# Kernel tuning notes

Hardware: AMD Instinct MI355X
Metric: run time of the kernel (lower is better)

## Reference

```python
import jax, jax.numpy as jnp
import numpy as np

H = 1024       # hidden_size
R = 4          # downsacale_ratio -> bottleneck H//R = 256
DI = 2048      # mamba d_inner = expand * H
NS = 16        # d_state
KC = 4         # d_conv
DTR = 64       # dt_rank = ceil(H/16)
B, L = 4, 1024


def setup_inputs() -> dict:
    key = jax.random.key(0)
    ks = iter(jax.random.split(key, 32))
    w = lambda shape, s=0.02: jax.random.normal(next(ks), shape, jnp.float32) * s
    Hr = H // R
    inp = {
        'x': jax.random.normal(next(ks), (B, L, H), jnp.float32),
        't': jax.random.normal(next(ks), (B, H), jnp.float32),
        # adaLN modulation: SiLU -> Linear(H, 3H)
        'ada_w': w((H, 3 * H)), 'ada_b': jnp.zeros((3 * H,), jnp.float32),
        # hg_dense: Linear(H,H/R) SiLU Linear(H/R,H)
        'hgd_w1': w((H, Hr)), 'hgd_b1': jnp.zeros((Hr,), jnp.float32),
        'hgd_w2': w((Hr, H)), 'hgd_b2': jnp.zeros((H,), jnp.float32),
        # Mamba params
        'in_proj_w': w((H, 2 * DI)),
        'conv_w': w((DI, KC), 0.1), 'conv_b': jnp.zeros((DI,), jnp.float32),
        'x_proj_w': w((DI, DTR + 2 * NS)),
        'dt_proj_w': w((DTR, DI), 0.1),
        'dt_proj_b': jnp.log(jnp.expm1(jnp.full((DI,), 0.01, jnp.float32))),  # softplus^-1(0.01)
        'A_log': jnp.log(jnp.broadcast_to(jnp.arange(1, NS + 1, dtype=jnp.float32), (DI, NS))),
        'Dp': jnp.ones((DI,), jnp.float32),
        'out_proj_w': w((DI, H)),
        # hg_fuse
        'fm_w': w((H, Hr)), 'fm_b': jnp.zeros((Hr,), jnp.float32),
        'fr_w': w((H, Hr)), 'fr_b': jnp.zeros((Hr,), jnp.float32),
        'ff_w': w((Hr, H)), 'ff_b': jnp.zeros((H,), jnp.float32),
    }
    return inp


def _ln(x, eps=1e-6):
    mu = jnp.mean(x, -1, keepdims=True)
    var = jnp.mean(jnp.square(x - mu), -1, keepdims=True)
    return (x - mu) / jnp.sqrt(var + eps)


def _mamba(xd, in_proj_w, conv_w, conv_b, x_proj_w, dt_proj_w, dt_proj_b, A_log, Dp, out_proj_w):
    # xd: [B, L, H]
    xz = xd @ in_proj_w                      # [B, L, 2*DI]
    xm, z = jnp.split(xz, 2, axis=-1)
    # causal depthwise conv over time
    xc = jnp.swapaxes(xm, 1, 2)              # [B, DI, L]
    xc = jax.lax.conv_general_dilated(
        xc, conv_w[:, None, :], window_strides=(1,), padding=[(KC - 1, 0)],
        feature_group_count=DI, dimension_numbers=('NCH', 'OIH', 'NCH'))
    xc = jax.nn.silu(jnp.swapaxes(xc, 1, 2) + conv_b)   # [B, L, DI]
    dbl = xc @ x_proj_w                      # [B, L, DTR + 2*NS]
    dt = jax.nn.softplus(dbl[..., :DTR] @ dt_proj_w + dt_proj_b)   # [B, L, DI]
    Bm = dbl[..., DTR:DTR + NS]              # [B, L, NS]
    Cm = dbl[..., DTR + NS:]                 # [B, L, NS]
    A = -jnp.exp(A_log)                      # [DI, NS]

    def step(h, inp):
        dt_t, x_t, B_t, C_t = inp            # [B,DI],[B,DI],[B,NS],[B,NS]
        dA = jnp.exp(dt_t[:, :, None] * A)                       # [B, DI, NS]
        h = dA * h + (dt_t * x_t)[:, :, None] * B_t[:, None, :]
        y = jnp.einsum('bdn,bn->bd', h, C_t)
        return h, y

    h0 = jnp.zeros((xd.shape[0], DI, NS), xd.dtype)
    seq = (jnp.moveaxis(dt, 1, 0), jnp.moveaxis(xc, 1, 0),
           jnp.moveaxis(Bm, 1, 0), jnp.moveaxis(Cm, 1, 0))
    _, ys = jax.lax.scan(step, h0, seq)
    y = jnp.moveaxis(ys, 0, 1) + xc * Dp     # [B, L, DI]
    y = y * jax.nn.silu(z)
    return y @ out_proj_w                    # [B, L, H]


def reference(x, t, ada_w, ada_b, hgd_w1, hgd_b1, hgd_w2, hgd_b2,
              in_proj_w, conv_w, conv_b, x_proj_w, dt_proj_w, dt_proj_b,
              A_log, Dp, out_proj_w, fm_w, fm_b, fr_w, fr_b, ff_w, ff_b):
    ada = jax.nn.silu(t) @ ada_w + ada_b               # [B, 3H]
    shift, scale, alpha = jnp.split(ada, 3, axis=-1)
    x1 = _ln(x) * (1 + scale[:, None, :]) + shift[:, None, :]
    xd = jax.nn.silu(x1 @ hgd_w1 + hgd_b1) @ hgd_w2 + hgd_b2
    x1_2 = _mamba(xd, in_proj_w, conv_w, conv_b, x_proj_w, dt_proj_w,
                  dt_proj_b, A_log, Dp, out_proj_w)
    a = jax.nn.silu(x1_2 @ fm_w + fm_b)
    b = jax.nn.silu(x1 @ fr_w + fr_b)
    fuse = (a * b) @ ff_w + ff_b
    return x + alpha[:, None, :] * fuse
```

## Files before the change

kernel.cpp:

```cpp
#include <hip/hip_runtime.h>
#include <math.h>
#include <stdint.h>

#define H_   1024
#define HR_  256
#define DI_  2048
#define NS_  16
#define KC_  4
#define DTR_ 64
#define B_   4
#define L_   1024
#define ROWS (B_*L_)
#define H3_  3072
#define NCH_ 16
#define CL_  64
#define CLT_ 8

typedef short bf16x8 __attribute__((ext_vector_type(8)));
typedef float f32x4  __attribute__((ext_vector_type(4)));

__device__ __forceinline__ float silu_f(float v) { return v / (1.f + __expf(-v)); }

__device__ __forceinline__ uint32_t pack_bf16_2(float a, float b) {
    uint32_t ua = __float_as_uint(a);
    uint32_t ub = __float_as_uint(b);
    uint32_t ra = (ua + 0x7FFFu + ((ua >> 16) & 1u)) >> 16;
    uint32_t rb = (ub + 0x7FFFu + ((ub >> 16) & 1u)) >> 16;
    return ra | (rb << 16);
}
__device__ __forceinline__ unsigned short cvt_bf16(float a) {
    uint32_t ua = __float_as_uint(a);
    return (unsigned short)((ua + 0x7FFFu + ((ua >> 16) & 1u)) >> 16);
}
__device__ __forceinline__ float bf16_to_f(unsigned short u) {
    return __uint_as_float(((uint32_t)u) << 16);
}

__device__ __forceinline__ void gload16(const short* g, short* l) {
    __builtin_amdgcn_global_load_lds(
        (const __attribute__((address_space(1))) void*)g,
        (__attribute__((address_space(3))) void*)l, 16, 0, 0);
}

#define TW_HGDFR 0ull
#define TW_HGD2  524288ull
#define TW_INPJ  786432ull
#define TW_XPJ   4980736ull
#define TW_DTPJ  5242880ull
#define TW_OPJ   5373952ull
#define TW_FM    7471104ull
#define TW_FF    7733248ull
#define TWT      7995392ull

__global__ __launch_bounds__(256) void wtrans_kernel(
    const float* __restrict__ s0, const float* __restrict__ s1,
    const float* __restrict__ s2, const float* __restrict__ s3,
    const float* __restrict__ s4, const float* __restrict__ s5,
    const float* __restrict__ s6, const float* __restrict__ s7,
    const float* __restrict__ s8, short* __restrict__ wt)
{
    int bid = blockIdx.x;
    const float* src; short* dst; int K, N, rel;
    if      (bid < 256)  { src = s0; dst = wt + TW_HGDFR;          K = 1024; N = 256;  rel = bid; }
    else if (bid < 512)  { src = s1; dst = wt + TW_HGDFR + 262144; K = 1024; N = 256;  rel = bid - 256; }
    else if (bid < 768)  { src = s2; dst = wt + TW_HGD2;           K = 256;  N = 1024; rel = bid - 512; }
    else if (bid < 4864) { src = s3; dst = wt + TW_INPJ;           K = 1024; N = 4096; rel = bid - 768; }
    else if (bid < 5120) { src = s4; dst = wt + TW_XPJ;            K = 2048; N = 96;   rel = bid - 4864; }
    else if (bid < 5248) { src = s5; dst = wt + TW_DTPJ;           K = 64;   N = 2048; rel = bid - 5120; }
    else if (bid < 7296) { src = s6; dst = wt + TW_OPJ;            K = 2048; N = 1024; rel = bid - 5248; }
    else if (bid < 7552) { src = s7; dst = wt + TW_FM;             K = 1024; N = 256;  rel = bid - 7296; }
    else                 { src = s8; dst = wt + TW_FF;             K = 256;  N = 1024; rel = bid - 7552; }
    int tkc = K >> 5;
    int tk = rel % tkc, tn = rel / tkc;

    __shared__ float ld[32][33];
    int tx = threadIdx.x & 7, ty = threadIdx.x >> 3;
    int kk = tk * 32 + ty, nn = tn * 32 + tx * 4;
    float4 v = make_float4(0.f, 0.f, 0.f, 0.f);
    if (nn < N) v = *(const float4*)&src[(size_t)kk * N + nn];
    ld[ty][tx * 4 + 0] = v.x; ld[ty][tx * 4 + 1] = v.y;
    ld[ty][tx * 4 + 2] = v.z; ld[ty][tx * 4 + 3] = v.w;
    __syncthreads();
    int nn2 = tn * 32 + ty, kk2 = tk * 32 + tx * 4;
    float a0 = ld[tx * 4 + 0][ty], a1 = ld[tx * 4 + 1][ty];
    float a2 = ld[tx * 4 + 2][ty], a3 = ld[tx * 4 + 3][ty];
    uint2 p = { pack_bf16_2(a0, a1), pack_bf16_2(a2, a3) };
    *(uint2*)&dst[(size_t)nn2 * K + kk2] = p;
}

__global__ __launch_bounds__(256) void cwt_kernel(
    const float* __restrict__ conv_w, float* __restrict__ cwt)
{
    int d = blockIdx.x * 256 + threadIdx.x;
    float4 v = *(const float4*)&conv_w[d * KC_];
    cwt[0 * DI_ + d] = v.x;
    cwt[1 * DI_ + d] = v.y;
    cwt[2 * DI_ + d] = v.z;
    cwt[3 * DI_ + d] = v.w;
}

__global__ __launch_bounds__(256) void ada_kernel(
    const float* __restrict__ t, const float* __restrict__ ada_w,
    const float* __restrict__ ada_b, float* __restrict__ ada)
{
    int b   = blockIdx.y;
    int col = blockIdx.x * 256 + threadIdx.x;
    __shared__ float st[H_];
    for (int i = threadIdx.x; i < H_; i += 256) {
        float v = t[b * H_ + i];
        st[i] = silu_f(v);
    }
    __syncthreads();
    float acc = 0.f;
    for (int k = 0; k < H_; ++k)
        acc = fmaf(st[k], ada_w[(size_t)k * H3_ + col], acc);
    ada[b * H3_ + col] = acc + ada_b[col];
}

__global__ __launch_bounds__(256) void ln_mod_kernel(
    const float* __restrict__ x, const float* __restrict__ ada,
    short* __restrict__ x1b)
{
    int row = blockIdx.x;
    int b   = row >> 10;
    const float* xr = x + (size_t)row * H_;
    float4 v = ((const float4*)xr)[threadIdx.x];
    float s  = v.x + v.y + v.z + v.w;
    float s2 = v.x*v.x + v.y*v.y + v.z*v.z + v.w*v.w;

    __shared__ float red[8];
    int wave = threadIdx.x >> 6, lane = threadIdx.x & 63;
    #pragma unroll
    for (int off = 32; off; off >>= 1) {
        s  += __shfl_down(s,  off);
        s2 += __shfl_down(s2, off);
    }
    if (lane == 0) { red[wave] = s; red[4 + wave] = s2; }
    __syncthreads();
    float ts  = red[0] + red[1] + red[2] + red[3];
    float ts2 = red[4] + red[5] + red[6] + red[7];
    float mu  = ts  * (1.f / H_);
    float var = ts2 * (1.f / H_) - mu * mu;
    float inv = rsqrtf(var + 1e-6f);

    const float* sh = ada + b * H3_;
    int i = threadIdx.x * 4;
    float4 sh4 = *(const float4*)&sh[i];
    float4 sc4 = *(const float4*)&sh[H_ + i];
    float ox = (v.x - mu) * inv * (1.f + sc4.x) + sh4.x;
    float oy = (v.y - mu) * inv * (1.f + sc4.y) + sh4.y;
    float oz = (v.z - mu) * inv * (1.f + sc4.z) + sh4.z;
    float ow = (v.w - mu) * inv * (1.f + sc4.w) + sh4.w;
    uint2 p = { pack_bf16_2(ox, oy), pack_bf16_2(oz, ow) };
    *(uint2*)(x1b + (size_t)row * H_ + i) = p;
}

template<int ACT, bool SPLITK>
__global__ __launch_bounds__(256) void gemm128(
    const short* __restrict__ A, int lda,
    const short* __restrict__ Wt, int ldw,
    const float* __restrict__ bias,
    float* __restrict__ C, short* __restrict__ Cb, short* __restrict__ Cb2,
    int ldc, int M, int N, int K,
    const float* __restrict__ E0, const float* __restrict__ E1)
{
    __shared__ short As[3][4096];
    __shared__ short Bs[3][4096];
    int tid  = threadIdx.x;
    int lane = tid & 63, wv = tid >> 6, wm = wv >> 1, wn = wv & 1;
    int n0 = blockIdx.x * 128;
    int m0 = blockIdx.y * 128;

    if (SPLITK) {
        int z = blockIdx.z;
        A  += (size_t)z * K;
        Wt += (size_t)z * K;
        C  += (size_t)z * M * N;
    }

    int r = lane & 15, g = lane >> 4;
    int sA = wv * 2;
    const short* ga0 = A  + (size_t)(m0 + sA * 16 + r) * lda + g * 8;
    const short* ga1 = ga0 + (size_t)16 * lda;
    const short* gb0 = Wt + (size_t)(n0 + sA * 16 + r) * ldw + g * 8;
    const short* gb1 = gb0 + (size_t)16 * ldw;

    f32x4 acc[4][4];
    #pragma unroll
    for (int i = 0; i < 4; ++i)
        #pragma unroll
        for (int j = 0; j < 4; ++j) {
            acc[i][j][0] = 0.f; acc[i][j][1] = 0.f;
            acc[i][j][2] = 0.f; acc[i][j][3] = 0.f;
        }

    #define STAGE(buf, koff)                                    \
        do {                                                    \
            gload16(ga0 + (koff), &As[buf][sA * 512]);          \
            gload16(ga1 + (koff), &As[buf][sA * 512 + 512]);    \
            gload16(gb0 + (koff), &Bs[buf][sA * 512]);          \
            gload16(gb1 + (koff), &Bs[buf][sA * 512 + 512]);    \
        } while (0)

    #define COMPUTE(buf)                                                          \
        do {                                                                      \
            bf16x8 af[4], bfr[4];                                                 \
            _Pragma("unroll")                                                     \
            for (int i = 0; i < 4; ++i)                                           \
                af[i] = *(const bf16x8*)&As[buf][(wm * 4 + i) * 512 + lane * 8];  \
            _Pragma("unroll")                                                     \
            for (int j = 0; j < 4; ++j)                                           \
                bfr[j] = *(const bf16x8*)&Bs[buf][(wn * 4 + j) * 512 + lane * 8]; \
            _Pragma("unroll")                                                     \
            for (int i = 0; i < 4; ++i)                                           \
                _Pragma("unroll")                                                 \
                for (int j = 0; j < 4; ++j)                                       \
                    acc[i][j] = __builtin_amdgcn_mfma_f32_16x16x32_bf16(          \
                        af[i], bfr[j], acc[i][j], 0, 0, 0);                       \
        } while (0)

    int T = K >> 5;
    STAGE(0, 0);
    if (T > 1) STAGE(1, 32);
    for (int t = 0; t < T; ++t) {
        if (t + 1 < T) asm volatile("s_waitcnt vmcnt(4)" ::: "memory");
        else           asm volatile("s_waitcnt vmcnt(0)" ::: "memory");
        __builtin_amdgcn_s_barrier();
        if (t + 2 < T) STAGE((t + 2) % 3, (t + 2) * 32);
        COMPUTE(t % 3);
    }
    #undef STAGE
    #undef COMPUTE

    #pragma unroll
    for (int i = 0; i < 4; ++i) {
        int mb = m0 + wm * 64 + i * 16 + ((lane >> 4) << 2);
        #pragma unroll
        for (int j = 0; j < 4; ++j) {
            int n = n0 + wn * 64 + j * 16 + (lane & 15);
            if (n < N) {
                float bv;
                if (ACT == 6) bv = (n < 256) ? bias[n] : E0[n - 256];
                else          bv = bias ? bias[n] : 0.f;
                #pragma unroll
                for (int rr = 0; rr < 4; ++rr) {
                    int m = mb + rr;
                    float v = acc[i][j][rr] + bv;
                    size_t ci = (size_t)m * ldc + n;
                    if (ACT == 6) {
                        float sv = silu_f(v);
                        if (n < 256) Cb[(size_t)m * 256 + n]        = (short)cvt_bf16(sv);
                        else         Cb2[(size_t)m * 256 + (n-256)] = (short)cvt_bf16(sv);
                    } else {
                        if (ACT == 2) v = (v > 20.f) ? v : log1pf(__expf(v));
                        else if (ACT == 4) {
                            int bb = m >> 10;
                            v = E0[ci] + E1[bb * H3_ + 2 * H_ + n] * v;
                        }
                        if (C)  C[ci]  = v;
                        if (Cb) Cb[ci] = (short)cvt_bf16(v);
                    }
                }
            }
        }
    }
}

template<int ACT>
__global__ __launch_bounds__(512) void gemm256(
    const short* __restrict__ A, int lda,
    const short* __restrict__ Wt, int ldw,
    short* __restrict__ Cb, int M, int N, int K)
{
    extern __shared__ short lds[];
    short* Asb = lds;
    short* Bsb = lds + 24576;
    int tid  = threadIdx.x;
    int lane = tid & 63, wv = tid >> 6;
    int wm = wv >> 2, wn = wv & 3;
    int n0 = blockIdx.x * 256;
    int m0 = blockIdx.y * 256;

    int r = lane & 15, g = lane >> 4;
    int sA = wv * 2;
    const short* ga0 = A  + (size_t)(m0 + sA * 16 + r) * lda + g * 8;
    const short* ga1 = ga0 + (size_t)16 * lda;
    const short* gb0 = Wt + (size_t)(n0 + sA * 16 + r) * ldw + g * 8;
    const short* gb1 = gb0 + (size_t)16 * ldw;

    f32x4 acc[8][4];
    #pragma unroll
    for (int i = 0; i < 8; ++i)
        #pragma unroll
        for (int j = 0; j < 4; ++j) {
            acc[i][j][0] = 0.f; acc[i][j][1] = 0.f;
            acc[i][j][2] = 0.f; acc[i][j][3] = 0.f;
        }

    #define STAGE2(buf, koff)                                       \
        do {                                                        \
            gload16(ga0 + (koff), &Asb[(buf) * 8192 + sA * 512]);   \
            gload16(ga1 + (koff), &Asb[(buf) * 8192 + sA * 512 + 512]); \
            gload16(gb0 + (koff), &Bsb[(buf) * 8192 + sA * 512]);   \
            gload16(gb1 + (koff), &Bsb[(buf) * 8192 + sA * 512 + 512]); \
        } while (0)

    int T = K >> 5;
    STAGE2(0, 0);
    if (T > 1) STAGE2(1, 32);
    for (int t = 0; t < T; ++t) {
        if (t + 1 < T) asm volatile("s_waitcnt vmcnt(4)" ::: "memory");
        else           asm volatile("s_waitcnt vmcnt(0)" ::: "memory");
        __builtin_amdgcn_s_barrier();
        if (t + 2 < T) STAGE2((t + 2) % 3, (t + 2) * 32);
        {
            int buf = t % 3;
            bf16x8 af[8], bfr[4];
            #pragma unroll
            for (int i = 0; i < 8; ++i)
                af[i] = *(const bf16x8*)&Asb[buf * 8192 + (wm * 8 + i) * 512 + lane * 8];
            #pragma unroll
            for (int j = 0; j < 4; ++j)
                bfr[j] = *(const bf16x8*)&Bsb[buf * 8192 + (wn * 4 + j) * 512 + lane * 8];
            __builtin_amdgcn_s_setprio(1);
            #pragma unroll
            for (int i = 0; i < 8; ++i)
                #pragma unroll
                for (int j = 0; j < 4; ++j)
                    acc[i][j] = __builtin_amdgcn_mfma_f32_16x16x32_bf16(
                        af[i], bfr[j], acc[i][j], 0, 0, 0);
            __builtin_amdgcn_s_setprio(0);
        }
    }
    #undef STAGE2

    #pragma unroll
    for (int i = 0; i < 8; ++i) {
        int mb = m0 + wm * 128 + i * 16 + ((lane >> 4) << 2);
        #pragma unroll
        for (int j = 0; j < 4; ++j) {
            int n = n0 + wn * 64 + j * 16 + (lane & 15);
            #pragma unroll
            for (int rr = 0; rr < 4; ++rr) {
                int m = mb + rr;
                float v = acc[i][j][rr];
                if (ACT == 5) {
                    size_t idx = (n < DI_) ? ((size_t)m * DI_ + n)
                                           : ((size_t)ROWS * DI_ + (size_t)m * DI_ + (n - DI_));
                    Cb[idx] = (short)cvt_bf16(v);
                }
            }
        }
    }
}

__global__ __launch_bounds__(256) void redk_xproj(
    const float* __restrict__ part, float* __restrict__ dbl,
    short* __restrict__ dblb)
{
    size_t i = ((size_t)blockIdx.x * 256 + threadIdx.x) * 4;
    const size_t seg = (size_t)ROWS * 96;
    float4 s = *(const float4*)(part + i);
    #pragma unroll
    for (int z = 1; z < 8; ++z) {
        float4 p = *(const float4*)(part + z * seg + i);
        s.x += p.x; s.y += p.y; s.z += p.z; s.w += p.w;
    }
    *(float4*)(dbl + i) = s;
    uint2 p = { pack_bf16_2(s.x, s.y), pack_bf16_2(s.z, s.w) };
    *(uint2*)(dblb + i) = p;
}

__global__ __launch_bounds__(256) void redk_op(
    const float* __restrict__ part, short* __restrict__ x12b)
{
    size_t i = ((size_t)blockIdx.x * 256 + threadIdx.x) * 4;
    const size_t seg = (size_t)ROWS * H_;
    float4 a = *(const float4*)(part + i);
    float4 b = *(const float4*)(part + seg + i);
    uint2 p = { pack_bf16_2(a.x + b.x, a.y + b.y), pack_bf16_2(a.z + b.z, a.w + b.w) };
    *(uint2*)(x12b + i) = p;
}

__global__ __launch_bounds__(256) void redk_fm(
    const float* __restrict__ part, const float* __restrict__ fm_b,
    const short* __restrict__ frlin, short* __restrict__ abb)
{
    size_t i = ((size_t)blockIdx.x * 256 + threadIdx.x) * 4;
    const size_t seg = (size_t)ROWS * HR_;
    float4 s = *(const float4*)(part + i);
    #pragma unroll
    for (int z = 1; z < 4; ++z) {
        float4 p = *(const float4*)(part + z * seg + i);
        s.x += p.x; s.y += p.y; s.z += p.z; s.w += p.w;
    }
    int col = (int)(i & (HR_ - 1));
    float4 b = *(const float4*)(fm_b + col);
    const short* fr = frlin + i;
    float o0 = silu_f(s.x + b.x) * bf16_to_f((unsigned short)fr[0]);
    float o1 = silu_f(s.y + b.y) * bf16_to_f((unsigned short)fr[1]);
    float o2 = silu_f(s.z + b.z) * bf16_to_f((unsigned short)fr[2]);
    float o3 = silu_f(s.w + b.w) * bf16_to_f((unsigned short)fr[3]);
    uint2 p = { pack_bf16_2(o0, o1), pack_bf16_2(o2, o3) };
    *(uint2*)(abb + i) = p;
}

__global__ __launch_bounds__(256) void conv_kernel(
    const short* __restrict__ xmb, const float* __restrict__ cwt,
    const float* __restrict__ conv_b, short* __restrict__ xcb)
{
    int d0 = threadIdx.x * 8;
    int b  = blockIdx.y;
    int l0 = blockIdx.x * CLT_;

    float w[KC_][8];
    #pragma unroll
    for (int j = 0; j < KC_; ++j) {
        float4 a = *(const float4*)&cwt[j * DI_ + d0];
        float4 c = *(const float4*)&cwt[j * DI_ + d0 + 4];
        w[j][0] = a.x; w[j][1] = a.y; w[j][2] = a.z; w[j][3] = a.w;
        w[j][4] = c.x; w[j][5] = c.y; w[j][6] = c.z; w[j][7] = c.w;
    }
    float bia[8];
    {
        float4 b0 = *(const float4*)&conv_b[d0];
        float4 b1 = *(const float4*)&conv_b[d0 + 4];
        bia[0] = b0.x; bia[1] = b0.y; bia[2] = b0.z; bia[3] = b0.w;
        bia[4] = b1.x; bia[5] = b1.y; bia[6] = b1.z; bia[7] = b1.w;
    }

    const short* base = xmb + (size_t)b * L_ * DI_ + d0;
    short*       outb = xcb + (size_t)b * L_ * DI_ + d0;

    bf16x8 win[KC_];
    #pragma unroll
    for (int j = 0; j < KC_ - 1; ++j) {
        int ll = l0 - (KC_ - 1) + j;
        if (ll >= 0) win[j] = *(const bf16x8*)(base + (size_t)ll * DI_);
        else         win[j] = (bf16x8)0;
    }
    for (int l = l0; l < l0 + CLT_; ++l) {
        win[KC_ - 1] = *(const bf16x8*)(base + (size_t)l * DI_);
        bf16x8 o;
        #pragma unroll
        for (int e = 0; e < 8; ++e) {
            float acc = bia[e];
            #pragma unroll
            for (int j = 0; j < KC_; ++j)
                acc = fmaf(bf16_to_f((unsigned short)win[j][e]), w[j][e], acc);
            o[e] = (short)cvt_bf16(silu_f(acc));
        }
        *(bf16x8*)(outb + (size_t)l * DI_) = o;
        win[0] = win[1]; win[1] = win[2]; win[2] = win[3];
    }
}

__global__ __launch_bounds__(256) void scan_part1(
    const short* __restrict__ dtb, const short* __restrict__ xcb,
    const float* __restrict__ dbl, const float* __restrict__ A_log,
    float* __restrict__ hend, float* __restrict__ dtsum)
{
    int bx = blockIdx.x;
    int dg = bx & 7;
    int bc = bx >> 3;
    int c  = bc & (NCH_ - 1);
    int b  = bc >> 4;
    int d  = dg * 256 + threadIdx.x;

    float Aa[NS_];
    #pragma unroll
    for (int n = 0; n < NS_; ++n) Aa[n] = -__expf(A_log[d * NS_ + n]);

    __shared__ float sB[CL_][NS_];
    for (int idx = threadIdx.x; idx < CL_ * NS_; idx += 256) {
        int l = idx >> 4, n = idx & 15;
        sB[l][n] = dbl[(size_t)(b * L_ + c * CL_ + l) * 96 + DTR_ + n];
    }
    __syncthreads();

    float h[NS_];
    #pragma unroll
    for (int n = 0; n < NS_; ++n) h[n] = 0.f;
    float sdt = 0.f;

    for (int l = 0; l < CL_; ++l) {
        size_t off = (size_t)(b * L_ + c * CL_ + l) * DI_ + d;
        float dtv = bf16_to_f((unsigned short)dtb[off]);
        float xv  = bf16_to_f((unsigned short)xcb[off]);
        float du  = dtv * xv;
        sdt += dtv;
        #pragma unroll
        for (int n = 0; n < NS_; ++n)
            h[n] = fmaf(__expf(dtv * Aa[n]), h[n], du * sB[l][n]);
    }
    #pragma unroll
    for (int n = 0; n < NS_; ++n)
        hend[((size_t)((b * NCH_ + c) * NS_ + n)) * DI_ + d] = h[n];
    dtsum[(size_t)(b * NCH_ + c) * DI_ + d] = sdt;
}

__global__ __launch_bounds__(256) void scan_part2(
    const short* __restrict__ dtb, const short* __restrict__ xcb,
    const short* __restrict__ zb, const float* __restrict__ dbl,
    const float* __restrict__ A_log, const float* __restrict__ Dp,
    const float* __restrict__ hend, const float* __restrict__ dtsum,
    short* __restrict__ y2b)
{
    int bx = blockIdx.x;
    int dg = bx & 7;
    int bc = bx >> 3;
    int c  = bc & (NCH_ - 1);
    int b  = bc >> 4;
    int d  = dg * 256 + threadIdx.x;

    float Aa[NS_];
    #pragma unroll
    for (int n = 0; n < NS_; ++n) Aa[n] = -__expf(A_log[d * NS_ + n]);

    __shared__ float sBC[CL_][2 * NS_];
    for (int idx = threadIdx.x; idx < CL_ * 2 * NS_; idx += 256) {
        int l = idx >> 5, n = idx & 31;
        sBC[l][n] = dbl[(size_t)(b * L_ + c * CL_ + l) * 96 + DTR_ + n];
    }
    __syncthreads();

    float h[NS_];
    #pragma unroll
    for (int n = 0; n < NS_; ++n) h[n] = 0.f;
    for (int j = 0; j < c; ++j) {
        float s = dtsum[(size_t)(b * NCH_ + j) * DI_ + d];
        #pragma unroll
        for (int n = 0; n < NS_; ++n)
            h[n] = fmaf(__expf(Aa[n] * s), h[n],
                        hend[((size_t)((b * NCH_ + j) * NS_ + n)) * DI_ + d]);
    }

    float Dpv = Dp[d];
    for (int l = 0; l < CL_; ++l) {
        size_t row = (size_t)(b * L_ + c * CL_ + l);
        size_t off = row * DI_ + d;
        float dtv = bf16_to_f((unsigned short)dtb[off]);
        float xv  = bf16_to_f((unsigned short)xcb[off]);
        float zv  = bf16_to_f((unsigned short)zb[off]);
        float du  = dtv * xv;
        float y = 0.f;
        #pragma unroll
        for (int n = 0; n < NS_; ++n) {
            float dA = __expf(dtv * Aa[n]);
            h[n] = fmaf(dA, h[n], du * sBC[l][n]);
            y = fmaf(h[n], sBC[l][NS_ + n], y);
        }
        y = fmaf(xv, Dpv, y);
        y2b[off] = (short)cvt_bf16(y * silu_f(zv));
    }
}

extern "C" void kernel_launch(void* const* d_in, const int* in_sizes, int n_in,
                              void* d_out, int out_size, void* d_ws, size_t ws_size,
                              hipStream_t stream)
{
    const float* x         = (const float*)d_in[0];
    const float* t         = (const float*)d_in[1];
    const float* ada_w     = (const float*)d_in[2];
    const float* ada_b     = (const float*)d_in[3];
    const float* hgd_w1    = (const float*)d_in[4];
    const float* hgd_b1    = (const float*)d_in[5];
    const float* hgd_w2    = (const float*)d_in[6];
    const float* hgd_b2    = (const float*)d_in[7];
    const float* in_proj_w = (const float*)d_in[8];
    const float* conv_w    = (const float*)d_in[9];
    const float* conv_b    = (const float*)d_in[10];
    const float* x_proj_w  = (const float*)d_in[11];
    const float* dt_proj_w = (const float*)d_in[12];
    const float* dt_proj_b = (const float*)d_in[13];
    const float* A_log     = (const float*)d_in[14];
    const float* Dp        = (const float*)d_in[15];
    const float* out_proj_w= (const float*)d_in[16];
    const float* fm_w      = (const float*)d_in[17];
    const float* fm_b      = (const float*)d_in[18];
    const float* fr_w      = (const float*)d_in[19];
    const float* fr_b      = (const float*)d_in[20];
    const float* ff_w      = (const float*)d_in[21];
    const float* ff_b      = (const float*)d_in[22];
    float* out = (float*)d_out;

    char* p = (char*)d_ws;
    auto alloc = [&](size_t bytes) { char* r = p; p += (bytes + 255) & ~255ull; return r; };

    short* wt      = (short*)alloc(TWT * 2);
    float* cwt     = (float*)alloc((size_t)KC_ * DI_ * 4);
    short* x1b     = (short*)alloc((size_t)ROWS * H_ * 2);
    short* h1b     = (short*)alloc((size_t)ROWS * HR_ * 2);
    short* frlin   = (short*)alloc((size_t)ROWS * HR_ * 2);
    short* xdb     = (short*)alloc((size_t)ROWS * H_ * 2);
    short* xmzb    = (short*)alloc((size_t)ROWS * DI_ * 4);
    short* xcb     = (short*)alloc((size_t)ROWS * DI_ * 2);
    short* y2b     = (short*)alloc((size_t)ROWS * DI_ * 2);
    short* dtb     = (short*)alloc((size_t)ROWS * DI_ * 2);
    float* bigpart = (float*)alloc((size_t)2 * ROWS * H_ * 4);
    float* dbl     = (float*)alloc((size_t)ROWS * 96 * 4);
    short* dblb    = (short*)alloc((size_t)ROWS * 96 * 2);
    short* x12b    = (short*)alloc((size_t)ROWS * H_ * 2);
    short* abb     = (short*)alloc((size_t)ROWS * HR_ * 2);
    float* ada     = (float*)alloc((size_t)B_ * H3_ * 4);

    short* xmb   = xmzb;
    short* zb    = xmzb + (size_t)ROWS * DI_;
    float* hend  = (float*)x12b;
    float* dtsum = (float*)abb;

    dim3 blk(256), b512(512);

    wtrans_kernel<<<dim3(7808), blk, 0, stream>>>(
        hgd_w1, fr_w, hgd_w2, in_proj_w, x_proj_w, dt_proj_w, out_proj_w,
        fm_w, ff_w, wt);
    cwt_kernel<<<dim3(DI_ / 256), blk, 0, stream>>>(conv_w, cwt);
    ada_kernel<<<dim3(H3_ / 256, B_), blk, 0, stream>>>(t, ada_w, ada_b, ada);
    ln_mod_kernel<<<dim3(ROWS), blk, 0, stream>>>(x, ada, x1b);
    gemm128<6, false><<<dim3(4, 32), blk, 0, stream>>>(
        x1b, H_, wt + TW_HGDFR, H_, hgd_b1, nullptr, h1b, frlin,
        512, ROWS, 512, H_, fr_b, nullptr);
    gemm128<0, false><<<dim3(8, 32), blk, 0, stream>>>(
        h1b, HR_, wt + TW_HGD2, HR_, hgd_b2, nullptr, xdb, nullptr,
        H_, ROWS, H_, HR_, nullptr, nullptr);
    gemm256<5><<<dim3(16, 16), b512, 98304, stream>>>(
        xdb, H_, wt + TW_INPJ, H_, xmb, ROWS, 2 * DI_, H_);
    conv_kernel<<<dim3(L_ / CLT_, B_), blk, 0, stream>>>(xmb, cwt, conv_b, xcb);
    gemm128<0, true><<<dim3(1, 32, 8), blk, 0, stream>>>(
        xcb, DI_, wt + TW_XPJ, DI_, nullptr, bigpart, nullptr, nullptr,
        96, ROWS, 96, 256, nullptr, nullptr);
    redk_xproj<<<dim3(ROWS * 96 / 4 / 256), blk, 0, stream>>>(bigpart, dbl, dblb);
    gemm128<2, false><<<dim3(16, 32), blk, 0, stream>>>(
        dblb, 96, wt + TW_DTPJ, DTR_, dt_proj_b, nullptr, dtb, nullptr,
        DI_, ROWS, DI_, DTR_, nullptr, nullptr);
    scan_part1<<<dim3(B_ * NCH_ * 8), blk, 0, stream>>>(
        dtb, xcb, dbl, A_log, hend, dtsum);
    scan_part2<<<dim3(B_ * NCH_ * 8), blk, 0, stream>>>(
        dtb, xcb, zb, dbl, A_log, Dp, hend, dtsum, y2b);
    gemm128<0, true><<<dim3(8, 32, 2), blk, 0, stream>>>(
        y2b, DI_, wt + TW_OPJ, DI_, nullptr, bigpart, nullptr, nullptr,
        H_, ROWS, H_, 1024, nullptr, nullptr);
    redk_op<<<dim3(ROWS * H_ / 4 / 256), blk, 0, stream>>>(bigpart, x12b);
    gemm128<0, true><<<dim3(2, 32, 4), blk, 0, stream>>>(
        x12b, H_, wt + TW_FM, H_, nullptr, bigpart, nullptr, nullptr,
        HR_, ROWS, HR_, 256, nullptr, nullptr);
    redk_fm<<<dim3(ROWS * HR_ / 4 / 256), blk, 0, stream>>>(bigpart, fm_b, frlin, abb);
    gemm128<4, false><<<dim3(8, 32), blk, 0, stream>>>(
        abb, HR_, wt + TW_FF, HR_, ff_b, out, nullptr, nullptr,
        H_, ROWS, H_, HR_, x, ada);
}
```

Baseline: 404.6 us.

## Split scan state across thread pairs and add a separate inter-chunk prefix kernel

The chunked selective scan now assigns two threads per channel, each owning 8 of the 16 state entries. This doubles the block count and halves per-thread register and exp work, and the two halves of y are combined with a shuffle. The sequential inter-chunk carry, which each part-2 block used to recompute over all earlier chunks, moves into a new scan_mid kernel that writes the starting state of every chunk once. The cost is an extra kernel launch, duplicated dt/x/z loads across each thread pair, and the hin buffer reusing bigpart memory.

Result: no change. 409.0 us (+1.1%).

```diff
diff --git a/kernel.cpp b/kernel.cpp
--- a/kernel.cpp
+++ b/kernel.cpp
@@ -461,15 +461,18 @@
     float* __restrict__ hend, float* __restrict__ dtsum)
 {
     int bx = blockIdx.x;
-    int dg = bx & 7;
-    int bc = bx >> 3;
+    int dg = bx & 15;
+    int bc = bx >> 4;
     int c  = bc & (NCH_ - 1);
     int b  = bc >> 4;
-    int d  = dg * 256 + threadIdx.x;
-
-    float Aa[NS_];
-    #pragma unroll
-    for (int n = 0; n < NS_; ++n) Aa[n] = -__expf(A_log[d * NS_ + n]);
+    int tid  = threadIdx.x;
+    int d    = dg * 128 + (tid >> 1);
+    int half = tid & 1;
+    int n0   = half * 8;
+
+    float Aa[8];
+    #pragma unroll
+    for (int n = 0; n < 8; ++n) Aa[n] = -__expf(A_log[d * NS_ + n0 + n]);
 
     __shared__ float sB[CL_][NS_];
     for (int idx = threadIdx.x; idx < CL_ * NS_; idx += 256) {
@@ -478,9 +481,9 @@
     }
     __syncthreads();
 
-    float h[NS_];
-    #pragma unroll
-    for (int n = 0; n < NS_; ++n) h[n] = 0.f;
+    float h[8];
+    #pragma unroll
+    for (int n = 0; n < 8; ++n) h[n] = 0.f;
     float sdt = 0.f;
 
     for (int l = 0; l < CL_; ++l) {
@@ -490,32 +493,55 @@
         float du  = dtv * xv;
         sdt += dtv;
         #pragma unroll
-        for (int n = 0; n < NS_; ++n)
-            h[n] = fmaf(__expf(dtv * Aa[n]), h[n], du * sB[l][n]);
-    }
-    #pragma unroll
-    for (int n = 0; n < NS_; ++n)
-        hend[((size_t)((b * NCH_ + c) * NS_ + n)) * DI_ + d] = h[n];
-    dtsum[(size_t)(b * NCH_ + c) * DI_ + d] = sdt;
+        for (int n = 0; n < 8; ++n)
+            h[n] = fmaf(__expf(dtv * Aa[n]), h[n], du * sB[l][n0 + n]);
+    }
+    #pragma unroll
+    for (int n = 0; n < 8; ++n)
+        hend[((size_t)((b * NCH_ + c) * NS_ + n0 + n)) * DI_ + d] = h[n];
+    if (half == 0)
+        dtsum[(size_t)(b * NCH_ + c) * DI_ + d] = sdt;
+}
+
+__global__ __launch_bounds__(256) void scan_mid(
+    const float* __restrict__ hend, const float* __restrict__ dtsum,
+    const float* __restrict__ A_log, float* __restrict__ hin)
+{
+    int idx = blockIdx.x * 256 + threadIdx.x;
+    int d  = idx & (DI_ - 1);
+    int bn = idx >> 11;
+    int n  = bn & (NS_ - 1);
+    int b  = bn >> 4;
+    float Aa = -__expf(A_log[d * NS_ + n]);
+    float h = 0.f;
+    #pragma unroll
+    for (int c = 0; c < NCH_; ++c) {
+        size_t o = ((size_t)((b * NCH_ + c) * NS_ + n)) * DI_ + d;
+        hin[o] = h;
+        float s = dtsum[(size_t)(b * NCH_ + c) * DI_ + d];
+        h = fmaf(__expf(Aa * s), h, hend[o]);
+    }
 }
 
 __global__ __launch_bounds__(256) void scan_part2(
     const short* __restrict__ dtb, const short* __restrict__ xcb,
     const short* __restrict__ zb, const float* __restrict__ dbl,
     const float* __restrict__ A_log, const float* __restrict__ Dp,
-    const float* __restrict__ hend, const float* __restrict__ dtsum,
-    short* __restrict__ y2b)
+    const float* __restrict__ hin, short* __restrict__ y2b)
 {
     int bx = blockIdx.x;
-    int dg = bx & 7;
-    int bc = bx >> 3;
+    int dg = bx & 15;
+    int bc = bx >> 4;
     int c  = bc & (NCH_ - 1);
     int b  = bc >> 4;
-    int d  = dg * 256 + threadIdx.x;
-
-    float Aa[NS_];
-    #pragma unroll
-    for (int n = 0; n < NS_; ++n) Aa[n] = -__expf(A_log[d * NS_ + n]);
+    int tid  = threadIdx.x;
+    int d    = dg * 128 + (tid >> 1);
+    int half = tid & 1;
+    int n0   = half * 8;
+
+    float Aa[8];
+    #pragma unroll
+    for (int n = 0; n < 8; ++n) Aa[n] = -__expf(A_log[d * NS_ + n0 + n]);
 
     __shared__ float sBC[CL_][2 * NS_];
     for (int idx = threadIdx.x; idx < CL_ * 2 * NS_; idx += 256) {
@@ -524,16 +550,10 @@
     }
     __syncthreads();
 
-    float h[NS_];
-    #pragma unroll
-    for (int n = 0; n < NS_; ++n) h[n] = 0.f;
-    for (int j = 0; j < c; ++j) {
-        float s = dtsum[(size_t)(b * NCH_ + j) * DI_ + d];
-        #pragma unroll
-        for (int n = 0; n < NS_; ++n)
-            h[n] = fmaf(__expf(Aa[n] * s), h[n],
-                        hend[((size_t)((b * NCH_ + j) * NS_ + n)) * DI_ + d]);
-    }
+    float h[8];
+    #pragma unroll
+    for (int n = 0; n < 8; ++n)
+        h[n] = hin[((size_t)((b * NCH_ + c) * NS_ + n0 + n)) * DI_ + d];
 
     float Dpv = Dp[d];
     for (int l = 0; l < CL_; ++l) {
@@ -545,13 +565,16 @@
         float du  = dtv * xv;
         float y = 0.f;
         #pragma unroll
-        for (int n = 0; n < NS_; ++n) {
+        for (int n = 0; n < 8; ++n) {
             float dA = __expf(dtv * Aa[n]);
-            h[n] = fmaf(dA, h[n], du * sBC[l][n]);
-            y = fmaf(h[n], sBC[l][NS_ + n], y);
-        }
-        y = fmaf(xv, Dpv, y);
-        y2b[off] = (short)cvt_bf16(y * silu_f(zv));
+            h[n] = fmaf(dA, h[n], du * sBC[l][n0 + n]);
+            y = fmaf(h[n], sBC[l][NS_ + n0 + n], y);
+        }
+        y += __shfl_xor(y, 1);
+        if (half == 0) {
+            y = fmaf(xv, Dpv, y);
+            y2b[off] = (short)cvt_bf16(y * silu_f(zv));
+        }
     }
 }
 
@@ -608,6 +631,7 @@
     short* zb    = xmzb + (size_t)ROWS * DI_;
     float* hend  = (float*)x12b;
     float* dtsum = (float*)abb;
+    float* hin   = bigpart;
 
     dim3 blk(256), b512(512);
 
@@ -633,10 +657,12 @@
     gemm128<2, false><<<dim3(16, 32), blk, 0, stream>>>(
         dblb, 96, wt + TW_DTPJ, DTR_, dt_proj_b, nullptr, dtb, nullptr,
         DI_, ROWS, DI_, DTR_, nullptr, nullptr);
-    scan_part1<<<dim3(B_ * NCH_ * 8), blk, 0, stream>>>(
+    scan_part1<<<dim3(B_ * NCH_ * 16), blk, 0, stream>>>(
         dtb, xcb, dbl, A_log, hend, dtsum);
-    scan_part2<<<dim3(B_ * NCH_ * 8), blk, 0, stream>>>(
-        dtb, xcb, zb, dbl, A_log, Dp, hend, dtsum, y2b);
+    scan_mid<<<dim3(B_ * DI_ * NS_ / 256), blk, 0, stream>>>(
+        hend, dtsum, A_log, hin);
+    scan_part2<<<dim3(B_ * NCH_ * 16), blk, 0, stream>>>(
+        dtb, xcb, zb, dbl, A_log, Dp, hin, y2b);
     gemm128<0, true><<<dim3(8, 32, 2), blk, 0, stream>>>(
         y2b, DI_, wt + TW_OPJ, DI_, nullptr, bigpart, nullptr, nullptr,
         H_, ROWS, H_, 1024, nullptr, nullptr);
```
